# Optimization experiments

Hardware: AMD Instinct MI355X
Metric: run time of the kernel (lower is better)

## Reference

```python
import jax, jax.numpy as jnp
import numpy as np
from jax import lax

WINDOW_SIZE = 11
C1 = 0.01 ** 2
C2 = 0.03 ** 2


def make_window(window_size: int) -> jnp.ndarray:
    # scipy.ndimage.gaussian_filter(np.ones(ws), sigma) with mode='reflect'
    # preserves constant inputs exactly, so gauss_1d == ones(ws).
    # outer(ones, ones) / sum -> uniform box window of weight 1/ws^2.
    return jnp.full((window_size, window_size), 1.0 / (window_size * window_size), dtype=jnp.float32)


def setup_inputs() -> dict:
    key = jax.random.key(0)
    k1, k2 = jax.random.split(key)
    B, C, D, H, W = 1, 1, 64, 512, 512
    x = jax.random.uniform(k1, (B, C, D, H, W), dtype=jnp.float32)
    y = jax.random.uniform(k2, (B, C, D, H, W), dtype=jnp.float32)
    window = make_window(WINDOW_SIZE)
    return {"x": x, "y": y, "window": window}


def _windowed_sum(imgs, window):
    # imgs: [N,1,H,W]; window: [ws,ws]. 'same' cross-correlation (window is symmetric).
    ws = window.shape[0]
    pad = ws // 2
    w = window[None, None, :, :]  # [O=1, I=1, ws, ws]
    return lax.conv_general_dilated(
        imgs, w, window_strides=(1, 1), padding=[(pad, pad), (pad, pad)],
        dimension_numbers=("NCHW", "OIHW", "NCHW"))


def reference(x, y, window):
    B, C, D, H, W = x.shape
    # Fold depth into the conv batch dim: every depth slice is an independent 2D SSIM.
    xs = x.transpose(0, 2, 1, 3, 4).reshape(B * D, C, H, W)
    ys = y.transpose(0, 2, 1, 3, 4).reshape(B * D, C, H, W)
    # Single batched conv over [x, y, x^2, y^2, x*y]
    stacked = jnp.concatenate([xs, ys, xs * xs, ys * ys, xs * ys], axis=0)
    conv = _windowed_sum(stacked, window)
    mu_x, mu_y, e_x2, e_y2, e_xy = jnp.split(conv, 5, axis=0)
    mu_x_sq = mu_x * mu_x
    mu_y_sq = mu_y * mu_y
    mu_xy = mu_x * mu_y
    sigma_x_sq = e_x2 - mu_x_sq
    sigma_y_sq = e_y2 - mu_y_sq
    sigma_xy = e_xy - mu_xy
    ssim_map = ((2.0 * mu_xy + C1) * (2.0 * sigma_xy + C2)) / (
        (mu_x_sq + mu_y_sq + C1) * (sigma_x_sq + sigma_y_sq + C2))
    # Per-slice means averaged over slices == global mean (all slices same size).
    return 1.0 - ssim_map.mean()
```

## Files before the change

### kernel.cpp

```cpp
#include <hip/hip_runtime.h>


constexpr int IMG   = 512;
constexpr int RB    = 16;
constexpr int BANDS = IMG / RB;
constexpr int NBLK  = 64 * BANDS;
constexpr float K1 = 1.4641f;
constexpr float K2 = 13.1769f;

__device__ __forceinline__ float shr1(float v) {
  return __int_as_float(__builtin_amdgcn_update_dpp(
      0, __float_as_int(v), 0x138, 0xF, 0xF, true));
}
__device__ __forceinline__ float shl1(float v) {
  return __int_as_float(__builtin_amdgcn_update_dpp(
      0, __float_as_int(v), 0x130, 0xF, 0xF, true));
}

__device__ __forceinline__ void gl16(const float* g, float* l) {
  __builtin_amdgcn_global_load_lds(
      (const __attribute__((address_space(1))) void*)g,
      (__attribute__((address_space(3))) void*)l, 16, 0, 0);
}

#define VW(n) do {                                                             \
    asm volatile("s_waitcnt vmcnt(%0)" :: "n"(n) : "memory");                  \
    __builtin_amdgcn_sched_barrier(0);                                         \
  } while (0)

template <bool ATOMIC>
__global__ __launch_bounds__(64, 1) void ssim_main(const float* __restrict__ x,
                                                   const float* __restrict__ y,
                                                   float* __restrict__ out_ws) {
  __shared__ float ring[3 * 2048];

  const int lane = threadIdx.x;
  const int bid  = blockIdx.x;
  const int xcd  = bid & 7;
  const int qq   = bid >> 3;
  const int z    = xcd * 8 + (qq >> 5);
  const int band = qq & 31;
  const int o0   = band * RB;
  const int gs   = o0 - 5;

  const float* xs = x + (size_t)z * IMG * IMG;
  const float* ys = y + (size_t)z * IMG * IMG;
  const int l4 = lane * 4;
  const int lw = lane * 8;

  float sX[8] = {}, sY[8] = {}, sXX[8] = {}, sYY[8] = {}, sXY[8] = {};
  float acc = 0.f;

  auto issue_c = [&](int slot) {
    const int gr  = gs + slot;
    const int grc = gr < 0 ? 0 : (gr > IMG - 1 ? IMG - 1 : gr);
    const int rb  = (slot % 3) * 2048;
    const float* gx = xs + grc * IMG + l4;
    const float* gy = ys + grc * IMG + l4;
    gl16(gx,       &ring[rb]);
    gl16(gx + 256, &ring[rb + 256]);
    gl16(gy,       &ring[rb + 512]);
    gl16(gy + 256, &ring[rb + 768]);
  };
  auto issue_o = [&](int slot) {
    const int gr  = gs + slot - 11;
    const int grc = gr < 0 ? 0 : (gr > IMG - 1 ? IMG - 1 : gr);
    const int rb  = (slot % 3) * 2048;
    const float* gx = xs + grc * IMG + l4;
    const float* gy = ys + grc * IMG + l4;
    gl16(gx,       &ring[rb + 1024]);
    gl16(gx + 256, &ring[rb + 1280]);
    gl16(gy,       &ring[rb + 1536]);
    gl16(gy + 256, &ring[rb + 1792]);
  };

  auto hwin = [&](const float (&S)[8], float (&B)[8]) {
    const float vm5  = shr1(S[3]);
    const float vm4  = shr1(S[4]);
    const float vm3  = shr1(S[5]);
    const float vm2  = shr1(S[6]);
    const float vm1  = shr1(S[7]);
    const float vp8  = shl1(S[0]);
    const float vp9  = shl1(S[1]);
    const float vp10 = shl1(S[2]);
    const float vp11 = shl1(S[3]);
    const float vp12 = shl1(S[4]);
    float s = (((vm5 + vm4) + (vm3 + vm2)) + ((vm1 + S[0]) + (S[1] + S[2]))) +
              ((S[3] + S[4]) + S[5]);
    B[0] = s;
    s += S[6]  - vm5;  B[1] = s;
    s += S[7]  - vm4;  B[2] = s;
    s += vp8   - vm3;  B[3] = s;
    s += vp9   - vm2;  B[4] = s;
    s += vp10  - vm1;  B[5] = s;
    s += vp11  - S[0]; B[6] = s;
    s += vp12  - S[1]; B[7] = s;
  };

  auto outp = [&]() {
    float bX[8], bY[8], bXX[8], bYY[8], bXY[8];
    hwin(sX, bX); hwin(sY, bY); hwin(sXX, bXX); hwin(sYY, bYY); hwin(sXY, bXY);
#pragma unroll
    for (int j = 0; j < 8; ++j) {
      const float bx  = bX[j];
      const float by  = bY[j];
      const float bxy = bx * by;
      const float sq  = fmaf(bx, bx, by * by);
      const float n1  = fmaf(2.f, bxy, K1);
      const float n2  = fmaf(242.f, bXY[j], fmaf(-2.f, bxy, K2));
      const float d1  = sq + K1;
      const float d2  = fmaf(121.f, bXX[j] + bYY[j], K2 - sq);
      acc += (n1 * n2) * __builtin_amdgcn_rcpf(d1 * d2);
    }
  };

  auto consumeW = [&](int slot) {
    const int rb = (slot % 3) * 2048;
    const float mc = ((unsigned)(gs + slot) < (unsigned)IMG) ? 1.f : 0.f;
    const float4 a = *(const float4*)&ring[rb + lw];
    const float4 b = *(const float4*)&ring[rb + lw + 4];
    const float4 c = *(const float4*)&ring[rb + 512 + lw];
    const float4 d = *(const float4*)&ring[rb + 512 + lw + 4];
    const float cx[8] = {a.x, a.y, a.z, a.w, b.x, b.y, b.z, b.w};
    const float cy[8] = {c.x, c.y, c.z, c.w, d.x, d.y, d.z, d.w};
#pragma unroll
    for (int j = 0; j < 8; ++j) {
      const float cxm = cx[j] * mc, cym = cy[j] * mc;
      sX[j] += cxm;
      sY[j] += cym;
      sXX[j] = fmaf(cx[j], cxm, sXX[j]);
      sYY[j] = fmaf(cy[j], cym, sYY[j]);
      sXY[j] = fmaf(cx[j], cym, sXY[j]);
    }
  };

  auto consumeS = [&](int slot) {
    const int rb = (slot % 3) * 2048;
    const float mc = ((unsigned)(gs + slot) < (unsigned)IMG) ? 1.f : 0.f;
    const float mo = (slot >= 11 && (gs + slot - 11) >= 0) ? 1.f : 0.f;
    const float4 a = *(const float4*)&ring[rb + lw];
    const float4 b = *(const float4*)&ring[rb + lw + 4];
    const float4 c = *(const float4*)&ring[rb + 512 + lw];
    const float4 d = *(const float4*)&ring[rb + 512 + lw + 4];
    const float4 e = *(const float4*)&ring[rb + 1024 + lw];
    const float4 f = *(const float4*)&ring[rb + 1024 + lw + 4];
    const float4 g = *(const float4*)&ring[rb + 1536 + lw];
    const float4 h = *(const float4*)&ring[rb + 1536 + lw + 4];
    const float cx[8] = {a.x, a.y, a.z, a.w, b.x, b.y, b.z, b.w};
    const float cy[8] = {c.x, c.y, c.z, c.w, d.x, d.y, d.z, d.w};
    const float ox[8] = {e.x, e.y, e.z, e.w, f.x, f.y, f.z, f.w};
    const float oy[8] = {g.x, g.y, g.z, g.w, h.x, h.y, h.z, h.w};
#pragma unroll
    for (int j = 0; j < 8; ++j) {
      const float cxm = cx[j] * mc, cym = cy[j] * mc;
      const float oxm = ox[j] * mo, oym = oy[j] * mo;
      sX[j] += cxm - oxm;
      sY[j] += cym - oym;
      sXX[j] = fmaf(cx[j], cxm, fmaf(-ox[j], oxm, sXX[j]));
      sYY[j] = fmaf(cy[j], cym, fmaf(-oy[j], oym, sYY[j]));
      sXY[j] = fmaf(cx[j], cym, fmaf(-ox[j], oym, sXY[j]));
    }
    outp();
  };

  issue_c(0);
  issue_c(1);
#pragma unroll 1
  for (int s = 0; s < 10; ++s) {
    issue_c(s + 2);
    VW(8);
    consumeW(s);
  }
  issue_o(10);
  issue_o(11);
  issue_c(12);
  issue_o(12);
  VW(12);
  consumeS(10);
#pragma unroll 1
  for (int s = 11; s <= 23; ++s) {
    issue_c(s + 2);
    issue_o(s + 2);
    VW(16);
    consumeS(s);
  }
  VW(8);
  consumeS(24);
  VW(0);
  consumeS(25);

#pragma unroll
  for (int off = 32; off > 0; off >>= 1) acc += __shfl_down(acc, off, 64);
  if (lane == 0) {
    if (ATOMIC) {
      atomicAdd(out_ws, acc);
    } else {
      out_ws[bid] = acc;
    }
  }
}

__global__ void ssim_finalize(const float* __restrict__ partials, int n,
                              float* __restrict__ out) {
  __shared__ float wsum[4];
  float acc = 0.f;
  for (int i = threadIdx.x; i < n; i += 256) acc += partials[i];
#pragma unroll
  for (int off = 32; off > 0; off >>= 1) acc += __shfl_down(acc, off, 64);
  if ((threadIdx.x & 63) == 0) wsum[threadIdx.x >> 6] = acc;
  __syncthreads();
  if (threadIdx.x == 0) {
    const float t = wsum[0] + wsum[1] + wsum[2] + wsum[3];
    out[0] = 1.0f - t * (1.0f / (64.0f * 512.0f * 512.0f));
  }
}

__global__ void ssim_zero(float* p) {
  if (threadIdx.x == 0) p[0] = 0.f;
}

__global__ void ssim_finalize_atomic(const float* __restrict__ accp,
                                     float* __restrict__ out) {
  if (threadIdx.x == 0)
    out[0] = 1.0f - accp[0] * (1.0f / (64.0f * 512.0f * 512.0f));
}

extern "C" void kernel_launch(void* const* d_in, const int* in_sizes, int n_in,
                              void* d_out, int out_size, void* d_ws, size_t ws_size,
                              hipStream_t stream) {
  const float* x = (const float*)d_in[0];
  const float* y = (const float*)d_in[1];
  float* out = (float*)d_out;

  dim3 grid(NBLK);
  dim3 block(64);

  if (ws_size >= (size_t)NBLK * sizeof(float)) {
    float* partials = (float*)d_ws;
    ssim_main<false><<<grid, block, 0, stream>>>(x, y, partials);
    ssim_finalize<<<1, 256, 0, stream>>>(partials, NBLK, out);
  } else {
    float* accp = (float*)d_ws;
    ssim_zero<<<1, 64, 0, stream>>>(accp);
    ssim_main<true><<<grid, block, 0, stream>>>(x, y, accp);
    ssim_finalize_atomic<<<1, 64, 0, stream>>>(accp, out);
  }
}
```

Before: 191.1 us.

## Keep 13-row LDS ring so outgoing rows are reused instead of reloaded

Before, each step fetched both the incoming row and the outgoing row (11 rows back) from global memory into a 3-slot LDS ring, so every row was read twice. Now the LDS ring holds 13 rows, and the outgoing row is read from the copy already in LDS. This halves global loads per block. The schedule also changes to consume-then-issue, with fewer outstanding loads in flight (vmcnt 4), which trades prefetch depth for less traffic. Larger LDS per block (52KB) may limit occupancy.

After: 202.3 us. +5.9%, slower.

```diff
diff --git a/kernel.cpp b/kernel.cpp
--- a/kernel.cpp
+++ b/kernel.cpp
@@ -5,6 +5,7 @@
 constexpr int RB    = 16;
 constexpr int BANDS = IMG / RB;
 constexpr int NBLK  = 64 * BANDS;
+constexpr int DSLOT = 13;
 constexpr float K1 = 1.4641f;
 constexpr float K2 = 13.1769f;
 
@@ -32,7 +33,7 @@
 __global__ __launch_bounds__(64, 1) void ssim_main(const float* __restrict__ x,
                                                    const float* __restrict__ y,
                                                    float* __restrict__ out_ws) {
-  __shared__ float ring[3 * 2048];
+  __shared__ float ring[DSLOT * 1024];
 
   const int lane = threadIdx.x;
   const int bid  = blockIdx.x;
@@ -54,24 +55,14 @@
   auto issue_c = [&](int slot) {
     const int gr  = gs + slot;
     const int grc = gr < 0 ? 0 : (gr > IMG - 1 ? IMG - 1 : gr);
-    const int rb  = (slot % 3) * 2048;
+    const int pos = slot >= DSLOT ? slot - DSLOT : slot;
+    const int rb  = pos * 1024;
     const float* gx = xs + grc * IMG + l4;
     const float* gy = ys + grc * IMG + l4;
     gl16(gx,       &ring[rb]);
     gl16(gx + 256, &ring[rb + 256]);
     gl16(gy,       &ring[rb + 512]);
     gl16(gy + 256, &ring[rb + 768]);
-  };
-  auto issue_o = [&](int slot) {
-    const int gr  = gs + slot - 11;
-    const int grc = gr < 0 ? 0 : (gr > IMG - 1 ? IMG - 1 : gr);
-    const int rb  = (slot % 3) * 2048;
-    const float* gx = xs + grc * IMG + l4;
-    const float* gy = ys + grc * IMG + l4;
-    gl16(gx,       &ring[rb + 1024]);
-    gl16(gx + 256, &ring[rb + 1280]);
-    gl16(gy,       &ring[rb + 1536]);
-    gl16(gy + 256, &ring[rb + 1792]);
   };
 
   auto hwin = [&](const float (&S)[8], float (&B)[8]) {
@@ -114,9 +105,10 @@
     }
   };
 
-  auto consumeW = [&](int slot) {
-    const int rb = (slot % 3) * 2048;
-    const float mc = ((unsigned)(gs + slot) < (unsigned)IMG) ? 1.f : 0.f;
+  auto consumeW = [&](int s) {
+    const int pos = s >= DSLOT ? s - DSLOT : s;
+    const int rb  = pos * 1024;
+    const float mc = ((unsigned)(gs + s) < (unsigned)IMG) ? 1.f : 0.f;
     const float4 a = *(const float4*)&ring[rb + lw];
     const float4 b = *(const float4*)&ring[rb + lw + 4];
     const float4 c = *(const float4*)&ring[rb + 512 + lw];
@@ -134,18 +126,22 @@
     }
   };
 
-  auto consumeS = [&](int slot) {
-    const int rb = (slot % 3) * 2048;
-    const float mc = ((unsigned)(gs + slot) < (unsigned)IMG) ? 1.f : 0.f;
-    const float mo = (slot >= 11 && (gs + slot - 11) >= 0) ? 1.f : 0.f;
+  auto consumeS = [&](int s) {
+    const int pos = s >= DSLOT ? s - DSLOT : s;
+    const int rb  = pos * 1024;
+    const int so  = s - 11;
+    const int poso = so >= DSLOT ? so - DSLOT : so;
+    const int ro  = poso * 1024;
+    const float mc = ((unsigned)(gs + s) < (unsigned)IMG) ? 1.f : 0.f;
+    const float mo = (gs + so >= 0) ? 1.f : 0.f;
     const float4 a = *(const float4*)&ring[rb + lw];
     const float4 b = *(const float4*)&ring[rb + lw + 4];
     const float4 c = *(const float4*)&ring[rb + 512 + lw];
     const float4 d = *(const float4*)&ring[rb + 512 + lw + 4];
-    const float4 e = *(const float4*)&ring[rb + 1024 + lw];
-    const float4 f = *(const float4*)&ring[rb + 1024 + lw + 4];
-    const float4 g = *(const float4*)&ring[rb + 1536 + lw];
-    const float4 h = *(const float4*)&ring[rb + 1536 + lw + 4];
+    const float4 e = *(const float4*)&ring[ro + lw];
+    const float4 f = *(const float4*)&ring[ro + lw + 4];
+    const float4 g = *(const float4*)&ring[ro + 512 + lw];
+    const float4 h = *(const float4*)&ring[ro + 512 + lw + 4];
     const float cx[8] = {a.x, a.y, a.z, a.w, b.x, b.y, b.z, b.w};
     const float cy[8] = {c.x, c.y, c.z, c.w, d.x, d.y, d.z, d.w};
     const float ox[8] = {e.x, e.y, e.z, e.w, f.x, f.y, f.z, f.w};
@@ -167,24 +163,24 @@
   issue_c(1);
 #pragma unroll 1
   for (int s = 0; s < 10; ++s) {
+    VW(4);
+    consumeW(s);
+    __builtin_amdgcn_sched_barrier(0);
     issue_c(s + 2);
-    VW(8);
-    consumeW(s);
-  }
-  issue_o(10);
-  issue_o(11);
+  }
+  VW(4);
+  consumeW(10);
+  outp();
+  __builtin_amdgcn_sched_barrier(0);
   issue_c(12);
-  issue_o(12);
-  VW(12);
-  consumeS(10);
 #pragma unroll 1
   for (int s = 11; s <= 23; ++s) {
+    VW(4);
+    consumeS(s);
+    __builtin_amdgcn_sched_barrier(0);
     issue_c(s + 2);
-    issue_o(s + 2);
-    VW(16);
-    consumeS(s);
-  }
-  VW(8);
+  }
+  VW(4);
   consumeS(24);
   VW(0);
   consumeS(25);
```
